# Optimization experiments

Measured on AMD Instinct MI355X. Metric: run time of the kernel, lower is better.

The kernel has to match this reference:

```python
import jax, jax.numpy as jnp
import numpy as np

# module hyperparameters (from init_kwargs)
RR = 8          # number of rotating time-trace slots
PFRAC = 0.3     # potentiation fraction
GMAX = 1.0
GMIN = 0.1
TAU = 100.0     # decay time constant
SPKRANGE = 512  # number of spikes per sample
SN = 128        # batch of samples
P, H, W = 2, 128, 128  # polarity, sensor height, sensor width (hard-coded in source)


def setup_inputs() -> dict:
    key = jax.random.key(0)
    kx, ky, kp, kt, ktt, kl = jax.random.split(key, 6)
    x = jax.random.randint(kx, (SN, SPKRANGE), 0, H)
    y = jax.random.randint(ky, (SN, SPKRANGE), 0, W)
    pol = jax.random.randint(kp, (SN, SPKRANGE), 0, P)
    event = jnp.stack([x, y, pol], axis=-1).astype(jnp.int32)  # [SN, SPK, 3] -> (x, y, polarity)
    # monotonically increasing spike timestamps (float path of event[:, :, 3])
    ts = jnp.sort(jax.random.uniform(kt, (SN, SPKRANGE), dtype=jnp.float32) * 5000.0, axis=1)
    tt = jax.random.randint(ktt, (SN, SPKRANGE), 0, RR).astype(jnp.int32)
    tt = tt.at[:, 0].set(0)  # first spike is written to slot 0, matching the torch init
    length = jax.random.randint(kl, (SN,), 1, SPKRANGE).astype(jnp.int32)
    return {"event": event, "ts": ts, "time_trace": tt, "length": length}


def _forward(event, ts, time_trace, length):
    sidx = jnp.arange(SN)
    T2G = jnp.zeros((SN, RR, P, H, W), dtype=ts.dtype)
    # initial spike deposit into slot 0
    x0, y0, p0 = event[:, 0, 0], event[:, 0, 1], event[:, 0, 2]
    T2G = T2G.at[sidx, 0, p0, x0, y0].add(PFRAC * (GMAX - GMIN))

    def step(T2G, xs):
        ev, dt, tprev, tcur, n = xs  # ev:[SN,3], dt:[SN], tprev/tcur:[SN], n: step index
        m = jnp.exp(dt / TAU)  # exp((t[N-1]-t[N])/TAU), dt <= 0
        # gather previous slot slice: [SN, P, H, W]
        prev = jnp.take_along_axis(T2G, tprev[:, None, None, None, None], axis=1)[:, 0]
        new = m[:, None, None, None] * (prev - GMIN) + GMIN  # decay toward GMIN
        # conditional scatter-add potentiation at the spiking pixel
        old = new[sidx, ev[:, 2], ev[:, 0], ev[:, 1]]
        add = jnp.where(length > n, PFRAC * (GMAX - old), 0.0)
        new = new.at[sidx, ev[:, 2], ev[:, 0], ev[:, 1]].add(add)
        # scatter the updated slice into the current slot
        T2G = T2G.at[sidx, tcur].set(new)
        return T2G, None

    xs = (jnp.moveaxis(event[:, 1:], 1, 0),      # [SPK-1, SN, 3]
          (ts[:, :-1] - ts[:, 1:]).T,            # [SPK-1, SN] time deltas (t[N-1]-t[N])
          time_trace[:, :-1].T,                  # previous slot per step
          time_trace[:, 1:].T,                   # current slot per step
          jnp.arange(1, SPKRANGE))               # step index N
    T2G, _ = jax.lax.scan(step, T2G, xs)
    # MaxPool3d((1,2,2), stride (1,2,2)) over (P, H, W)
    pooled = T2G.reshape(SN, RR, P, H // 2, 2, W // 2, 2).max(axis=(4, 6))
    return pooled  # [SN, RR, 2, 64, 64]


def reference(event, ts, time_trace, length):
    return _forward(event, ts, time_trace, length)
```

## Files before the change

### kernel.cpp

```cpp
#include <hip/hip_runtime.h>

#define SN 128
#define SPK 512

constexpr float GMIN  = 0.1f;
constexpr float PFRAC = 0.3f;
constexpr float GMAX  = 1.0f;


__global__ __launch_bounds__(64, 2) void trace_kernel(
    const int*   __restrict__ event,
    const float* __restrict__ ts,
    const int*   __restrict__ tt,
    const int*   __restrict__ length,
    float*       __restrict__ out)
{
    const int wg   = blockIdx.x;
    const int s    = wg >> 4;
    const int p    = (wg >> 3) & 1;
    const int xq   = wg & 7;
    const int lane = threadIdx.x;

    const int   len = length[s];
    const float ts0 = ts[s * SPK];

    int tv[8]; float tsn[8]; int ex[8], ey[8], ep[8];
#pragma unroll
    for (int r8 = 0; r8 < 8; ++r8) {
        int n = r8 * 64 + lane;
        tv[r8]  = tt[s * SPK + n];
        tsn[r8] = ts[s * SPK + n];
        const int* ev = event + (size_t)(s * SPK + n) * 3;
        ex[r8] = ev[0]; ey[r8] = ev[1]; ep[r8] = ev[2];
    }

    int snl[8];
#pragma unroll
    for (int r = 0; r < 8; ++r) snl[r] = -1;
#pragma unroll
    for (int r8 = 0; r8 < 8; ++r8) {
        int n = r8 * 64 + lane;
#pragma unroll
        for (int r = 0; r < 8; ++r) {
            unsigned long long m = __ballot(n >= 1 && tv[r8] == r);
            if (m) snl[r] = r8 * 64 + 63 - __clzll(m);
        }
    }

    const int xp     = lane >> 3;
    const int yb     = lane & 7;
    const int x_even = xq * 16 + 2 * xp;
    const unsigned mypatO = (unsigned)((p << 14) | (x_even << 7) | (yb << 4)) | 0x8000u;
    const int Xo = xq * 8 + xp;

    float a[32];
#pragma unroll
    for (int j = 0; j < 32; ++j) a[j] = -GMIN;

    bool own0 = false; int j0 = 0;
    {
        const int* ev0 = event + (size_t)s * SPK * 3;
        int x0 = ev0[0], y0 = ev0[1], p0 = ev0[2];
        unsigned pos0 = (unsigned)((p0 << 14) | (x0 << 7) | y0);
        if ((pos0 & 0x7F70u) == (mypatO & 0x7F70u)) {
            own0 = true;
            j0 = ((x0 & 1) << 4) | (y0 & 15);
#pragma unroll
            for (int j = 0; j < 32; ++j)
                if (j == j0) a[j] = PFRAC * (GMAX - GMIN) - GMIN;
        }
    }

#pragma unroll
    for (int r8 = 0; r8 < 8; ++r8) {
        int n = r8 * 64 + lane;

        bool psnap = false;
#pragma unroll
        for (int r = 0; r < 8; ++r) psnap |= (n == snl[r]);
        bool powner = (n >= 1) && (n < len) && (ep[r8] == p) && ((ex[r8] >> 4) == xq);
        bool pred   = powner || psnap;

        unsigned mymw = 0u; float myC = 0.0f, myCr = 0.0f;
        if (pred) {
            float d = (ts0 - tsn[r8]) * 0.01f;
            myC  = __expf(d);
            myCr = (PFRAC * (GMAX - GMIN)) * __expf(-d);
            mymw = (unsigned)tv[r8] << 24;
            if (powner) {
                unsigned pos = (unsigned)((p << 14) | (ex[r8] << 7) | ey[r8]);
                mymw |= 0x8000u | (pos & 0x7F70u)
                      | ((unsigned)(((ex[r8] & 1) << 4) | (ey[r8] & 15)) << 16);
            }
            if (psnap) mymw |= 0x80000000u;
        }

        unsigned long long mask = __ballot(pred);
        while (mask) {
            int src = (int)__builtin_ctzll(mask);
            mask &= mask - 1;
            unsigned mw  = (unsigned)__builtin_amdgcn_readlane((int)mymw, src);
            int      Cri = __builtin_amdgcn_readlane(__float_as_int(myCr), src);

            bool  own  = (mw & 0xFF70u) == mypatO;
            float coef = own ? (1.0f - PFRAC) : 1.0f;
            float addb = own ? __int_as_float(Cri) : 0.0f;
            switch ((mw >> 16) & 31u) {
#define OWN_CASE(k) case k: a[k] = fmaf(coef, a[k], addb); break;
                OWN_CASE(0)  OWN_CASE(1)  OWN_CASE(2)  OWN_CASE(3)
                OWN_CASE(4)  OWN_CASE(5)  OWN_CASE(6)  OWN_CASE(7)
                OWN_CASE(8)  OWN_CASE(9)  OWN_CASE(10) OWN_CASE(11)
                OWN_CASE(12) OWN_CASE(13) OWN_CASE(14) OWN_CASE(15)
                OWN_CASE(16) OWN_CASE(17) OWN_CASE(18) OWN_CASE(19)
                OWN_CASE(20) OWN_CASE(21) OWN_CASE(22) OWN_CASE(23)
                OWN_CASE(24) OWN_CASE(25) OWN_CASE(26) OWN_CASE(27)
                OWN_CASE(28) OWN_CASE(29) OWN_CASE(30) OWN_CASE(31)
#undef OWN_CASE
            }

            if ((int)mw < 0) {
                int   Ci = __builtin_amdgcn_readlane(__float_as_int(myC), src);
                float C  = __int_as_float(Ci);
                int   rr = (int)((mw >> 24) & 7u);
                float o[8];
#pragma unroll
                for (int k = 0; k < 8; ++k) {
                    float v0 = fmaf(C, a[2 * k],      GMIN);
                    float v1 = fmaf(C, a[2 * k + 1],  GMIN);
                    float v2 = fmaf(C, a[16 + 2 * k], GMIN);
                    float v3 = fmaf(C, a[17 + 2 * k], GMIN);
                    o[k] = fmaxf(fmaxf(v0, v1), fmaxf(v2, v3));
                }
                float* dst = out +
                    (size_t)((((s * 8 + rr) * 2 + p) * 64 + Xo) * 64 + yb * 8);
                *reinterpret_cast<float4*>(dst)     = make_float4(o[0], o[1], o[2], o[3]);
                *reinterpret_cast<float4*>(dst + 4) = make_float4(o[4], o[5], o[6], o[7]);
            }
        }
    }

#pragma unroll
    for (int r = 0; r < 8; ++r) {
        if (snl[r] < 0) {
            float o[8];
#pragma unroll
            for (int k = 0; k < 8; ++k) {
                bool hit = (r == 0) && own0 && (k == ((j0 & 15) >> 1));
                o[k] = hit ? PFRAC * (GMAX - GMIN) : 0.0f;
            }
            float* dst = out +
                (size_t)((((s * 8 + r) * 2 + p) * 64 + Xo) * 64 + yb * 8);
            *reinterpret_cast<float4*>(dst)     = make_float4(o[0], o[1], o[2], o[3]);
            *reinterpret_cast<float4*>(dst + 4) = make_float4(o[4], o[5], o[6], o[7]);
        }
    }
}

extern "C" void kernel_launch(void* const* d_in, const int* in_sizes, int n_in,
                              void* d_out, int out_size, void* d_ws, size_t ws_size,
                              hipStream_t stream) {
    const int*   event  = (const int*)  d_in[0];
    const float* ts     = (const float*)d_in[1];
    const int*   tt     = (const int*)  d_in[2];
    const int*   length = (const int*)  d_in[3];
    float*       out    = (float*)d_out;

    trace_kernel<<<dim3(SN * 2 * 8), dim3(64), 0, stream>>>(event, ts, tt, length, out);
}
```

Measured before the change: 18.67 us.

## Compact active events into shared-memory list and stream with prefetched uniform loads

Active events (owner or snapshot) are no longer walked per 64-lane chunk through a ballot/readlane loop. Each one is first compacted by prefix popcount into a shared-memory array of packed metadata and coefficients. The main loop then iterates over that dense list with a two-entry prefetch, using readfirstlane for uniform values, and the last-writer search per slot scans chunks from the end with early exit. This is meant to cut per-event readlane and ballot overhead and loop control, at the cost of shared-memory traffic and an added compaction pass.

Result: slower. 27.92 us (+49.5%).

```diff
diff --git a/kernel.cpp b/kernel.cpp
--- a/kernel.cpp
+++ b/kernel.cpp
@@ -15,6 +15,8 @@
     const int*   __restrict__ length,
     float*       __restrict__ out)
 {
+    __shared__ uint4 sent[SPK + 10];
+
     const int wg   = blockIdx.x;
     const int s    = wg >> 4;
     const int p    = (wg >> 3) & 1;
@@ -24,33 +26,69 @@
     const int   len = length[s];
     const float ts0 = ts[s * SPK];
 
-    int tv[8]; float tsn[8]; int ex[8], ey[8], ep[8];
+    unsigned meta[8]; float tsn[8];
 #pragma unroll
     for (int r8 = 0; r8 < 8; ++r8) {
         int n = r8 * 64 + lane;
-        tv[r8]  = tt[s * SPK + n];
+        int tv_ = tt[s * SPK + n];
         tsn[r8] = ts[s * SPK + n];
         const int* ev = event + (size_t)(s * SPK + n) * 3;
-        ex[r8] = ev[0]; ey[r8] = ev[1]; ep[r8] = ev[2];
+        int ex = ev[0], ey = ev[1], ep = ev[2];
+        unsigned mw = (unsigned)tv_ << 24;
+        bool ownerb = (n >= 1) && (n < len) && (ep == p) && ((ex >> 4) == xq);
+        if (ownerb) {
+            mw |= 0x8000u
+                | ((unsigned)((p << 14) | (ex << 7) | ey) & 0x7F70u)
+                | ((unsigned)(((ex & 1) << 4) | (ey & 15)) << 16);
+        }
+        meta[r8] = mw;
     }
 
     int snl[8];
 #pragma unroll
-    for (int r = 0; r < 8; ++r) snl[r] = -1;
+    for (int r = 0; r < 8; ++r) {
+        int f = -1;
+#pragma unroll
+        for (int rr = 7; rr >= 0; --rr) {
+            if (f < 0) {
+                unsigned long long m =
+                    __ballot(((meta[rr] >> 24) & 7u) == (unsigned)r &&
+                             (rr > 0 || lane > 0));
+                if (m) f = rr * 64 + 63 - __clzll(m);
+            }
+        }
+        snl[r] = f;
+    }
+
+    const unsigned long long lmask = (1ull << lane) - 1ull;
+    int base = 0;
 #pragma unroll
     for (int r8 = 0; r8 < 8; ++r8) {
         int n = r8 * 64 + lane;
+        unsigned mw = meta[r8];
+        bool psnap = false;
 #pragma unroll
-        for (int r = 0; r < 8; ++r) {
-            unsigned long long m = __ballot(n >= 1 && tv[r8] == r);
-            if (m) snl[r] = r8 * 64 + 63 - __clzll(m);
+        for (int r = 0; r < 8; ++r) psnap |= (n == snl[r]);
+        bool pred = psnap || ((mw >> 15) & 1u);
+
+        unsigned long long bmask = __ballot(pred);
+        if (pred) {
+            float d  = (ts0 - tsn[r8]) * 0.01f;
+            float C  = __expf(d);
+            float Cr = (PFRAC * (GMAX - GMIN)) * __expf(-d);
+            if (psnap) mw |= 0x80000000u;
+            int idx = base + (int)__popcll(bmask & lmask);
+            sent[idx] = make_uint4(mw, __float_as_uint(C), __float_as_uint(Cr), 0u);
         }
+        base += (int)__popcll(bmask);
     }
+    const int cnt = base;
+    if (lane < 2) sent[cnt + lane] = make_uint4(0u, 0u, 0u, 0u);
 
     const int xp     = lane >> 3;
     const int yb     = lane & 7;
     const int x_even = xq * 16 + 2 * xp;
-    const unsigned mypatO = (unsigned)((p << 14) | (x_even << 7) | (yb << 4)) | 0x8000u;
+    const unsigned mypat = (unsigned)((p << 14) | (x_even << 7) | (yb << 4));
     const int Xo = xq * 8 + xp;
 
     float a[32];
@@ -62,7 +100,7 @@
         const int* ev0 = event + (size_t)s * SPK * 3;
         int x0 = ev0[0], y0 = ev0[1], p0 = ev0[2];
         unsigned pos0 = (unsigned)((p0 << 14) | (x0 << 7) | y0);
-        if ((pos0 & 0x7F70u) == (mypatO & 0x7F70u)) {
+        if ((pos0 & 0x7F70u) == mypat) {
             own0 = true;
             j0 = ((x0 & 1) << 4) | (y0 & 15);
 #pragma unroll
@@ -71,40 +109,17 @@
         }
     }
 
-#pragma unroll
-    for (int r8 = 0; r8 < 8; ++r8) {
-        int n = r8 * 64 + lane;
+    uint4 e0 = sent[0];
+    uint4 e1 = sent[1];
+    for (int i = 0; i < cnt; ++i) {
+        uint4 e2 = sent[i + 2];
+        unsigned mw = (unsigned)__builtin_amdgcn_readfirstlane((int)e0.x);
 
-        bool psnap = false;
-#pragma unroll
-        for (int r = 0; r < 8; ++r) psnap |= (n == snl[r]);
-        bool powner = (n >= 1) && (n < len) && (ep[r8] == p) && ((ex[r8] >> 4) == xq);
-        bool pred   = powner || psnap;
-
-        unsigned mymw = 0u; float myC = 0.0f, myCr = 0.0f;
-        if (pred) {
-            float d = (ts0 - tsn[r8]) * 0.01f;
-            myC  = __expf(d);
-            myCr = (PFRAC * (GMAX - GMIN)) * __expf(-d);
-            mymw = (unsigned)tv[r8] << 24;
-            if (powner) {
-                unsigned pos = (unsigned)((p << 14) | (ex[r8] << 7) | ey[r8]);
-                mymw |= 0x8000u | (pos & 0x7F70u)
-                      | ((unsigned)(((ex[r8] & 1) << 4) | (ey[r8] & 15)) << 16);
-            }
-            if (psnap) mymw |= 0x80000000u;
-        }
-
-        unsigned long long mask = __ballot(pred);
-        while (mask) {
-            int src = (int)__builtin_ctzll(mask);
-            mask &= mask - 1;
-            unsigned mw  = (unsigned)__builtin_amdgcn_readlane((int)mymw, src);
-            int      Cri = __builtin_amdgcn_readlane(__float_as_int(myCr), src);
-
-            bool  own  = (mw & 0xFF70u) == mypatO;
+        if (mw & 0x8000u) {
+            float Crs  = __int_as_float(__builtin_amdgcn_readfirstlane((int)e0.z));
+            bool  own  = (mw & 0x7F70u) == mypat;
             float coef = own ? (1.0f - PFRAC) : 1.0f;
-            float addb = own ? __int_as_float(Cri) : 0.0f;
+            float addb = own ? Crs : 0.0f;
             switch ((mw >> 16) & 31u) {
 #define OWN_CASE(k) case k: a[k] = fmaf(coef, a[k], addb); break;
                 OWN_CASE(0)  OWN_CASE(1)  OWN_CASE(2)  OWN_CASE(3)
@@ -117,26 +132,27 @@
                 OWN_CASE(28) OWN_CASE(29) OWN_CASE(30) OWN_CASE(31)
 #undef OWN_CASE
             }
+        }
 
-            if ((int)mw < 0) {
-                int   Ci = __builtin_amdgcn_readlane(__float_as_int(myC), src);
-                float C  = __int_as_float(Ci);
-                int   rr = (int)((mw >> 24) & 7u);
-                float o[8];
+        if ((int)mw < 0) {
+            float C  = __int_as_float(__builtin_amdgcn_readfirstlane((int)e0.y));
+            int   rr = (int)((mw >> 24) & 7u);
+            float o[8];
 #pragma unroll
-                for (int k = 0; k < 8; ++k) {
-                    float v0 = fmaf(C, a[2 * k],      GMIN);
-                    float v1 = fmaf(C, a[2 * k + 1],  GMIN);
-                    float v2 = fmaf(C, a[16 + 2 * k], GMIN);
-                    float v3 = fmaf(C, a[17 + 2 * k], GMIN);
-                    o[k] = fmaxf(fmaxf(v0, v1), fmaxf(v2, v3));
-                }
-                float* dst = out +
-                    (size_t)((((s * 8 + rr) * 2 + p) * 64 + Xo) * 64 + yb * 8);
-                *reinterpret_cast<float4*>(dst)     = make_float4(o[0], o[1], o[2], o[3]);
-                *reinterpret_cast<float4*>(dst + 4) = make_float4(o[4], o[5], o[6], o[7]);
+            for (int k = 0; k < 8; ++k) {
+                float v0 = fmaf(C, a[2 * k],      GMIN);
+                float v1 = fmaf(C, a[2 * k + 1],  GMIN);
+                float v2 = fmaf(C, a[16 + 2 * k], GMIN);
+                float v3 = fmaf(C, a[17 + 2 * k], GMIN);
+                o[k] = fmaxf(fmaxf(fmaxf(v0, v1), v2), v3);
             }
+            float* dst = out +
+                (size_t)((((s * 8 + rr) * 2 + p) * 64 + Xo) * 64 + yb * 8);
+            *reinterpret_cast<float4*>(dst)     = make_float4(o[0], o[1], o[2], o[3]);
+            *reinterpret_cast<float4*>(dst + 4) = make_float4(o[4], o[5], o[6], o[7]);
         }
+        e0 = e1;
+        e1 = e2;
     }
 
 #pragma unroll
```
